# Kernel optimization log

Measured on AMD Instinct MI355X. Metric: run time of the kernel, lower is better.

The kernel has to match this reference:

```python
import jax, jax.numpy as jnp
import numpy as np
from jax import lax

B, DIM, H, W = 2, 128, 192, 192
GS = [16, 32, 32, 48]          # group ratios [1,2,2,3]/8 of DIM
HID = int(DIM * 2.66)          # 340, Restormer-style hidden width


def _pool_mat(n_in, n_out):
    # torch AdaptiveAvgPool as an explicit linear map [n_out, n_in]
    P = np.zeros((n_out, n_in), np.float32)
    for o in range(n_out):
        s = (o * n_in) // n_out
        e = ((o + 1) * n_in + n_out - 1) // n_out
        P[o, s:e] = 1.0 / (e - s)
    return jnp.asarray(P)


def _ln(t, w, b):
    # WithBias LayerNorm over the channel dim of NCHW (== LN over last dim of b(hw)c)
    mu = t.mean(1, keepdims=True)
    var = ((t - mu) ** 2).mean(1, keepdims=True)
    return (t - mu) / jnp.sqrt(var + 1e-5) * w[None, :, None, None] + b[None, :, None, None]


def _c1x1(t, w):
    return jnp.einsum('oc,bchw->bohw', w, t)


def _dw3(t, w):
    return lax.conv_general_dilated(t, w, (1, 1), 'SAME',
                                    dimension_numbers=('NCHW', 'OIHW', 'NCHW'),
                                    feature_group_count=t.shape[1])


def _c1d(t, w, b):
    return jnp.einsum('oc,bcl->bol', w, t) + b[None, :, None]


def _gelu(t):
    return jax.nn.gelu(t, approximate=False)


def _forward(x, qv_cache, ln1_w, ln1_b, ln2_w, ln2_b, temperature, w_qkv, w_qkv_dw, w_proj,
             intra_down_w, intra_down_b, intra_up_w, intra_up_b, intra_gate_w, intra_gate_b,
             inter0_cw_w, inter0_cw_b, inter0_g_w, inter0_g_b,
             inter1_cw_w, inter1_cw_b, inter1_g_w, inter1_g_b,
             inter2_cw_w, inter2_cw_b, inter2_g_w, inter2_g_b,
             inter3_cw_w, inter3_cw_b, inter3_g_w, inter3_g_b,
             ffn_in_w, ffn_dw_w, ffn_out_w):
    b, c, h, w_ = x.shape
    hw = h * w_
    inter_p = [(inter0_cw_w, inter0_cw_b, inter0_g_w, inter0_g_b),
               (inter1_cw_w, inter1_cw_b, inter1_g_w, inter1_g_b),
               (inter2_cw_w, inter2_cw_b, inter2_g_w, inter2_g_b),
               (inter3_cw_w, inter3_cw_b, inter3_g_w, inter3_g_b)]
    # ---- attention branch ----
    xn = _ln(x, ln1_w, ln1_b)
    qkv = _dw3(_c1x1(xn, w_qkv), w_qkv_dw)
    q, k, v = jnp.split(qkv, 3, axis=1)
    q = q.reshape(b, c, hw); k = k.reshape(b, c, hw); v = v.reshape(b, c, hw)
    # correlation-based channel re-grouping (torch.corrcoef on batch-mean of q)
    cf = q.mean(0)                                   # [C, HW]
    xm = cf - cf.mean(1, keepdims=True)
    cov = xm @ xm.T
    dsd = jnp.sqrt(jnp.diagonal(cov))
    corr = cov / (dsd[:, None] * dsd[None, :])
    idx = jnp.argsort(-corr.mean(1))                 # descending mean similarity
    q = q[:, idx]; k = k[:, idx]; v = v[:, idx]
    atts, tmpc, outs = [], [], []
    start = 0
    for i, g in enumerate(GS):
        qg = q[:, start:start + g]; kg = k[:, start:start + g]; vg = v[:, start:start + g]
        start += g
        qn = qg / jnp.maximum(jnp.linalg.norm(qg, axis=-1, keepdims=True), 1e-12)
        kn = kg / jnp.maximum(jnp.linalg.norm(kg, axis=-1, keepdims=True), 1e-12)
        att = jax.nn.softmax(jnp.einsum('bcl,bdl->bcd', qn, kn) * temperature[i, 0, 0], axis=-1)
        tmpc.append(lax.stop_gradient(qn) + lax.stop_gradient(kn))
        # Inter_CacheModulation: adaptive-pool cache to [g,g], FiLM + gated conv1d
        cw_w, cw_b, g_w, g_b = inter_p[i]
        P = _pool_mat(c, g)
        aligned = jnp.einsum('oi,bij,pj->bop', P, qv_cache, P)    # [1, g, g]
        scale, shift = jnp.split(_c1d(aligned + att, cw_w, cw_b), 2, axis=1)
        x1p = att * scale + shift
        att = x1p * _gelu(_c1d(x1p, g_w, g_b)) + att
        atts.append(att)
        outs.append(jnp.einsum('bcd,bdl->bcl', att, vg))
    # CalculateCurrentLayerCache: resize each group's batch-mean attn to [C,C].
    # Original does (u * c_i) // dim with c_i == dim, i.e. elementwise floor.
    acc = jnp.zeros((1, c, c), x.dtype)
    for a in atts:
        m = lax.stop_gradient(a).mean(0, keepdims=True)[:, None]  # [1,1,g,g]
        u = jax.image.resize(m, (1, 1, c, c), method='bilinear')
        acc = acc + jnp.floor(u)[:, 0]
    qv_new = qv_cache * 0.9 + acc * 0.1
    out_all = jnp.concatenate(outs, axis=1)          # [B, C, HW]
    tmp_all = jnp.concatenate(tmpc, axis=1)
    # Intra_CacheModulation
    s = tmp_all + out_all
    gated = _gelu(_c1d(s, intra_gate_w, intra_gate_b)) * s
    out_all = _c1d(_c1d(gated, intra_down_w, intra_down_b), intra_up_w, intra_up_b) + out_all
    x1 = x + _c1x1(out_all.reshape(b, c, h, w_), w_proj)
    # ---- gated-dconv FFN ----
    xn2 = _ln(x1, ln2_w, ln2_b)
    y1, y2 = jnp.split(_dw3(_c1x1(xn2, ffn_in_w), ffn_dw_w), 2, axis=1)
    out = x1 + _c1x1(_gelu(y1) * y2, ffn_out_w)
    return out, qv_new


def setup_inputs() -> dict:
    key = jax.random.key(0)
    ks = jax.random.split(key, 40)
    def w(i, shape, s=0.02):
        return jax.random.normal(ks[i], shape, jnp.float32) * s
    p = {}
    p['x'] = jax.random.normal(ks[0], (B, DIM, H, W), jnp.float32)
    p['qv_cache'] = jax.random.uniform(ks[1], (1, DIM, DIM), jnp.float32)
    p['ln1_w'] = jnp.ones((DIM,), jnp.float32); p['ln1_b'] = jnp.zeros((DIM,), jnp.float32)
    p['ln2_w'] = jnp.ones((DIM,), jnp.float32); p['ln2_b'] = jnp.zeros((DIM,), jnp.float32)
    p['temperature'] = jnp.ones((4, 1, 1), jnp.float32)
    p['w_qkv'] = w(2, (3 * DIM, DIM))
    p['w_qkv_dw'] = w(3, (3 * DIM, 1, 3, 3))
    p['w_proj'] = w(4, (DIM, DIM))
    p['intra_down_w'] = w(5, (DIM // 2, DIM)); p['intra_down_b'] = jnp.zeros((DIM // 2,), jnp.float32)
    p['intra_up_w'] = w(6, (DIM, DIM // 2)); p['intra_up_b'] = jnp.zeros((DIM,), jnp.float32)
    p['intra_gate_w'] = w(7, (DIM, DIM)); p['intra_gate_b'] = jnp.zeros((DIM,), jnp.float32)
    for i, g in enumerate(GS):
        p[f'inter{i}_cw_w'] = w(8 + 2 * i, (2 * g, g))
        p[f'inter{i}_cw_b'] = jnp.zeros((2 * g,), jnp.float32)
        p[f'inter{i}_g_w'] = w(9 + 2 * i, (g, g))
        p[f'inter{i}_g_b'] = jnp.zeros((g,), jnp.float32)
    p['ffn_in_w'] = w(20, (2 * HID, DIM))
    p['ffn_dw_w'] = w(21, (2 * HID, 1, 3, 3))
    p['ffn_out_w'] = w(22, (DIM, HID))
    return p


def reference(x, qv_cache, ln1_w, ln1_b, ln2_w, ln2_b, temperature, w_qkv, w_qkv_dw, w_proj,
              intra_down_w, intra_down_b, intra_up_w, intra_up_b, intra_gate_w, intra_gate_b,
              inter0_cw_w, inter0_cw_b, inter0_g_w, inter0_g_b,
              inter1_cw_w, inter1_cw_b, inter1_g_w, inter1_g_b,
              inter2_cw_w, inter2_cw_b, inter2_g_w, inter2_g_b,
              inter3_cw_w, inter3_cw_b, inter3_g_w, inter3_g_b,
              ffn_in_w, ffn_dw_w, ffn_out_w):
    return _forward(x, qv_cache, ln1_w, ln1_b, ln2_w, ln2_b, temperature, w_qkv, w_qkv_dw, w_proj,
                    intra_down_w, intra_down_b, intra_up_w, intra_up_b, intra_gate_w, intra_gate_b,
                    inter0_cw_w, inter0_cw_b, inter0_g_w, inter0_g_b,
                    inter1_cw_w, inter1_cw_b, inter1_g_w, inter1_g_b,
                    inter2_cw_w, inter2_cw_b, inter2_g_w, inter2_g_b,
                    inter3_cw_w, inter3_cw_b, inter3_g_w, inter3_g_b,
                    ffn_in_w, ffn_dw_w, ffn_out_w)
```

## Files before the change

### kernel.cpp

```cpp
#include <hip/hip_runtime.h>
#include <math.h>

#define TPB 256

constexpr int BN_  = 2;
constexpr int CDIM = 128;
constexpr int HH   = 192;
constexpr int WW   = 192;
constexpr int HWc  = HH * WW;
constexpr int C3   = 384;
constexpr int HID  = 340;
constexpr int NL2  = 288;
constexpr int CH2  = HWc / NL2;
constexpr int CV   = 288;

typedef unsigned short bf16_t;
typedef __attribute__((ext_vector_type(8))) __bf16 bf16x8;
typedef __attribute__((ext_vector_type(4))) float f32x4;

__device__ __forceinline__ float b2f(bf16_t v) {
  unsigned u = ((unsigned)v) << 16;
  return __uint_as_float(u);
}
__device__ __forceinline__ bf16_t f2b(float f) {
  unsigned u = __float_as_uint(f);
  unsigned r = (u + 0x7FFFu + ((u >> 16) & 1u)) >> 16;
  return (bf16_t)r;
}
__device__ __forceinline__ float ldf(const float* p) { return *p; }
__device__ __forceinline__ float ldf(const bf16_t* p) { return b2f(*p); }
__device__ __forceinline__ void stf(float* p, float v) { *p = v; }
__device__ __forceinline__ void stf(bf16_t* p, float v) { *p = f2b(v); }

__device__ __forceinline__ void ldv4(const float* p, float* v) {
  float4 t = *(const float4*)p;
  v[0] = t.x; v[1] = t.y; v[2] = t.z; v[3] = t.w;
}
__device__ __forceinline__ void ldv4(const bf16_t* p, float* v) {
  ushort4 t = *(const ushort4*)p;
  v[0] = b2f(t.x); v[1] = b2f(t.y); v[2] = b2f(t.z); v[3] = b2f(t.w);
}
__device__ __forceinline__ void stv4(float* p, const float* v) {
  float4 t; t.x = v[0]; t.y = v[1]; t.z = v[2]; t.w = v[3];
  *(float4*)p = t;
}
__device__ __forceinline__ void stv4(bf16_t* p, const float* v) {
  ushort4 t; t.x = f2b(v[0]); t.y = f2b(v[1]); t.z = f2b(v[2]); t.w = f2b(v[3]);
  *(ushort4*)p = t;
}

__device__ __forceinline__ float gelu_f(float x) {
  return 0.5f * x * (1.0f + erff(x * 0.7071067811865475f));
}

__device__ __forceinline__ void unpack8(uint4 v, float* rv) {
  unsigned wv[4] = {v.x, v.y, v.z, v.w};
#pragma unroll
  for (int j = 0; j < 8; ++j)
    rv[j + 1] = b2f((bf16_t)((wv[j >> 1] >> ((j & 1) * 16)) & 0xFFFFu));
}
__device__ __forceinline__ uint4 pack8(const float* a) {
  uint4 o;
  unsigned w[4];
#pragma unroll
  for (int p = 0; p < 4; ++p) {
    unsigned lo = f2b(a[2 * p]), hi = f2b(a[2 * p + 1]);
    w[p] = lo | (hi << 16);
  }
  o.x = w[0]; o.y = w[1]; o.z = w[2]; o.w = w[3];
  return o;
}
__device__ __forceinline__ float sum8(uint4 v) {
  unsigned w[4] = {v.x, v.y, v.z, v.w};
  float s = 0.f;
#pragma unroll
  for (int j = 0; j < 8; ++j)
    s += b2f((bf16_t)((w[j >> 1] >> ((j & 1) * 16)) & 0xFFFFu));
  return s;
}
__device__ __forceinline__ float sumsq8(uint4 v) {
  unsigned w[4] = {v.x, v.y, v.z, v.w};
  float s = 0.f;
#pragma unroll
  for (int j = 0; j < 8; ++j) {
    float t = b2f((bf16_t)((w[j >> 1] >> ((j & 1) * 16)) & 0xFFFFu));
    s += t * t;
  }
  return s;
}

__device__ __constant__ int dGSZ[4]   = {16, 32, 32, 48};
__device__ __constant__ int dGST[4]   = {0, 16, 48, 80};
__device__ __constant__ int dAOFF[4]  = {0, 256, 1280, 2304};
__device__ __constant__ int dABASE[4] = {0, 512, 2560, 4608};

constexpr size_t oATTRAW  = 0;
constexpr size_t oATTS2   = 65536;
constexpr size_t oMUP     = 102400;
constexpr size_t oWB      = 131072;
constexpr size_t oATTS    = 1327104;
constexpr size_t oNORMQ   = 1363968;
constexpr size_t oNORMK   = 1364992;
constexpr size_t oIDX     = 1366016;
constexpr size_t oMU      = 1366528;
constexpr size_t oCOV     = 1367040;
constexpr size_t oQKV     = 1572864;
constexpr size_t oXN      = 58195968;
constexpr size_t oOUTALL  = 77070336;
constexpr size_t oSBUF    = 95944704;
constexpr size_t WS_NEED  = 114819072;
constexpr size_t oCHUNK1  = oOUTALL;
constexpr size_t oCOVPART = oOUTALL;
constexpr size_t oCOVP2   = oSBUF;
constexpr size_t oQKPART  = oXN;
constexpr size_t oGATED   = oQKV;
constexpr size_t oDBUF    = oQKV + 18874368;
constexpr size_t oY0C     = oOUTALL;
constexpr size_t oZ       = oQKV;
constexpr size_t oX1B     = oXN;

constexpr int eWQ   = 0;
constexpr int eGATE = 49152;
constexpr int eDOWN = 65536;
constexpr int eUP   = 73728;
constexpr int ePROJ = 81920;
constexpr int eFFI  = 98304;
constexpr int eFFO  = 185344;
constexpr int eTOT  = 234496;

__global__ __launch_bounds__(TPB) void k_wcvt(const float* __restrict__ wq,
                                              const float* __restrict__ gate,
                                              const float* __restrict__ down,
                                              const float* __restrict__ up,
                                              const float* __restrict__ proj,
                                              const float* __restrict__ ffi,
                                              const float* __restrict__ ffo,
                                              bf16_t* __restrict__ wb) {
  int t = blockIdx.x * TPB + threadIdx.x;
  if (t >= eTOT) return;
  int u = t;
  if (u < 49152) { wb[eWQ + u] = f2b(wq[u]); return; }
  u -= 49152;
  if (u < 16384) { wb[eGATE + u] = f2b(gate[u]); return; }
  u -= 16384;
  if (u < 8192)  { wb[eDOWN + u] = f2b(down[u]); return; }
  u -= 8192;
  if (u < 8192)  { wb[eUP + u] = f2b(up[u]); return; }
  u -= 8192;
  if (u < 16384) { wb[ePROJ + u] = f2b(proj[u]); return; }
  u -= 16384;
  if (u < 87040) { wb[eFFI + u] = f2b(ffi[u]); return; }
  u -= 87040;
  {
    int o = u / 384, k = u - o * 384;
    wb[eFFO + u] = (k < HID) ? f2b(ffo[o * HID + k]) : (bf16_t)0;
  }
}

template <typename TI>
__global__ __launch_bounds__(TPB) void k_ln(const TI* __restrict__ x,
                                            const float* __restrict__ w,
                                            const float* __restrict__ bias,
                                            bf16_t* __restrict__ out) {
  int t = blockIdx.x * TPB + threadIdx.x;
  if (t >= BN_ * HWc) return;
  int b = t / HWc, l = t - b * HWc;
  const TI* xb = x + (size_t)b * CDIM * HWc + l;
  float s = 0.f, s2 = 0.f;
#pragma unroll 4
  for (int c = 0; c < CDIM; ++c) { float v = ldf(&xb[(size_t)c * HWc]); s += v; s2 += v * v; }
  float mu  = s * (1.f / CDIM);
  float var = s2 * (1.f / CDIM) - mu * mu;
  float inv = 1.f / sqrtf(var + 1e-5f);
  bf16_t* ob = out + (size_t)b * CDIM * HWc + l;
#pragma unroll 4
  for (int c = 0; c < CDIM; ++c)
    stf(&ob[(size_t)c * HWc], (ldf(&xb[(size_t)c * HWc]) - mu) * inv * w[c] + bias[c]);
}

template <typename TO, typename TA, int KT, int EPI>
__global__ __launch_bounds__(TPB) void k_mgA(const bf16_t* __restrict__ W,
                                             const bf16_t* __restrict__ W2, int osplit,
                                             const float* __restrict__ bias,
                                             const bf16_t* __restrict__ in,
                                             const TA* __restrict__ aux,
                                             TO* __restrict__ out, int O,
                                             int ibr, int obr, int abr) {
  constexpr int L  = HWc;
  constexpr int PK = KT + 8;
  constexpr int KH = KT / 2;
  constexpr int SH = (KT == 128) ? 6 : 5;
  __shared__ bf16_t At[128 * PK];
  __shared__ bf16_t Wt[64 * PK];
  int b = blockIdx.y;
  const bf16_t* inb  = in  + (size_t)b * ibr * L;
  const TA*     auxb = aux ? aux + (size_t)b * abr * L : nullptr;
  TO*           outb = out + (size_t)b * obr * L;
  int l0 = blockIdx.x * 128;
  int tid = threadIdx.x, lane = tid & 63, wid = tid >> 6;
  int wm = wid >> 1, wn = wid & 1;
  int cl = lane & 15, rg = lane >> 4;

#pragma unroll
  for (int r = 0; r < (KH * 16) / TPB; ++r) {
    int u  = tid + r * TPB;
    int k2 = u & (KH - 1), lb = u >> SH;
    int ka = k2 * 2;
    uint4 rowA = *(const uint4*)(&inb[(size_t)ka * L + l0 + lb * 8]);
    uint4 rowB = *(const uint4*)(&inb[(size_t)(ka + 1) * L + l0 + lb * 8]);
    unsigned wa[4] = {rowA.x, rowA.y, rowA.z, rowA.w};
    unsigned wb[4] = {rowB.x, rowB.y, rowB.z, rowB.w};
#pragma unroll
    for (int j = 0; j < 8; ++j) {
      unsigned va = (wa[j >> 1] >> ((j & 1) * 16)) & 0xFFFFu;
      unsigned vb = (wb[j >> 1] >> ((j & 1) * 16)) & 0xFFFFu;
      *(unsigned*)(&At[(lb * 8 + j) * PK + ka]) = va | (vb << 16);
    }
  }

  int noc = (O + 63) >> 6;
  for (int oc = 0; oc < noc; ++oc) {
    int o0 = oc * 64;
#pragma unroll
    for (int r = 0; r < (64 * KT / 8) / TPB; ++r) {
      int e = tid + r * TPB;
      int o = e / (KT / 8), k8 = (e % (KT / 8)) * 8;
      int og = o0 + o;
      uint4 wv = {0u, 0u, 0u, 0u};
      if (og < O) {
        const bf16_t* wrow = (og < osplit) ? (W + (size_t)og * KT)
                                           : (W2 + (size_t)(og - osplit) * KT);
        wv = *(const uint4*)(&wrow[k8]);
      }
      *(uint4*)(&Wt[o * PK + k8]) = wv;
    }
    __syncthreads();
    f32x4 acc[2][4];
#pragma unroll
    for (int m = 0; m < 2; ++m)
#pragma unroll
      for (int n = 0; n < 4; ++n) acc[m][n] = (f32x4){0.f, 0.f, 0.f, 0.f};
#pragma unroll
    for (int kk = 0; kk < KT / 32; ++kk) {
      int kof = kk * 32 + rg * 8;
      bf16x8 a[2], bfr[4];
#pragma unroll
      for (int m = 0; m < 2; ++m)
        a[m] = *(const bf16x8*)(&Wt[(wm * 32 + m * 16 + cl) * PK + kof]);
#pragma unroll
      for (int n = 0; n < 4; ++n)
        bfr[n] = *(const bf16x8*)(&At[(wn * 64 + n * 16 + cl) * PK + kof]);
#pragma unroll
      for (int m = 0; m < 2; ++m)
#pragma unroll
        for (int n = 0; n < 4; ++n)
          acc[m][n] = __builtin_amdgcn_mfma_f32_16x16x32_bf16(bfr[n], a[m], acc[m][n], 0, 0, 0);
    }
    __syncthreads();
#pragma unroll
    for (int m = 0; m < 2; ++m) {
      int og = o0 + wm * 32 + m * 16 + cl;
      if (og >= O) continue;
      float bv = bias ? bias[og] : 0.f;
#pragma unroll
      for (int n = 0; n < 4; ++n) {
        int lcol = l0 + wn * 64 + n * 16 + rg * 4;
        size_t off = (size_t)og * L + lcol;
        float v[4];
#pragma unroll
        for (int r = 0; r < 4; ++r) v[r] = acc[m][n][r] + bv;
        if (EPI == 1) {
          float a4[4]; ldv4(&auxb[off], a4);
#pragma unroll
          for (int r = 0; r < 4; ++r) v[r] += a4[r];
        } else if (EPI == 2) {
          float a4[4]; ldv4(&auxb[off], a4);
#pragma unroll
          for (int r = 0; r < 4; ++r) v[r] = gelu_f(v[r]) * a4[r];
        }
        stv4(&outb[off], v);
      }
    }
  }
}

template <typename TO, typename TA, int EPI>
__global__ __launch_bounds__(TPB) void k_mgB(const bf16_t* __restrict__ Wb,
                                             const float* __restrict__ bias,
                                             const bf16_t* __restrict__ in,
                                             const TA* __restrict__ aux,
                                             TO* __restrict__ out, int O, int K,
                                             int ibr, int obr, int abr) {
  constexpr int L = HWc;
  constexpr int PK = 72, BK = 64, WSTR = 384;
  __shared__ bf16_t At[128 * PK];
  __shared__ bf16_t Wt[128 * PK];
  int b = blockIdx.y;
  const bf16_t* inb  = in  + (size_t)b * ibr * L;
  const TA*     auxb = aux ? aux + (size_t)b * abr * L : nullptr;
  TO*           outb = out + (size_t)b * obr * L;
  int l0 = blockIdx.x * 128;
  int tid = threadIdx.x, lane = tid & 63, wid = tid >> 6;
  int wm = wid >> 1, wn = wid & 1;
  int cl = lane & 15, rg = lane >> 4;

  f32x4 acc[4][4];
#pragma unroll
  for (int m = 0; m < 4; ++m)
#pragma unroll
    for (int n = 0; n < 4; ++n) acc[m][n] = (f32x4){0.f, 0.f, 0.f, 0.f};

  for (int k0 = 0; k0 < K; k0 += BK) {
#pragma unroll
    for (int r = 0; r < 2; ++r) {
      int u = tid + r * TPB;
      int k2 = u & 31, lb = u >> 5;
      int ka = k0 + k2 * 2;
      uint4 rowA = {0u,0u,0u,0u}, rowB = {0u,0u,0u,0u};
      if (ka < K)     rowA = *(const uint4*)(&inb[(size_t)ka * L + l0 + lb * 8]);
      if (ka + 1 < K) rowB = *(const uint4*)(&inb[(size_t)(ka + 1) * L + l0 + lb * 8]);
      unsigned wa[4] = {rowA.x, rowA.y, rowA.z, rowA.w};
      unsigned wb[4] = {rowB.x, rowB.y, rowB.z, rowB.w};
#pragma unroll
      for (int j = 0; j < 8; ++j) {
        unsigned va = (wa[j >> 1] >> ((j & 1) * 16)) & 0xFFFFu;
        unsigned vb = (wb[j >> 1] >> ((j & 1) * 16)) & 0xFFFFu;
        *(unsigned*)(&At[(lb * 8 + j) * PK + k2 * 2]) = va | (vb << 16);
      }
    }
#pragma unroll
    for (int r = 0; r < 4; ++r) {
      int e = tid + r * TPB;
      int o = e >> 3, k8 = (e & 7) * 8;
      uint4 wv = *(const uint4*)(&Wb[(size_t)o * WSTR + k0 + k8]);
      *(uint4*)(&Wt[o * PK + k8]) = wv;
    }
    __syncthreads();
#pragma unroll
    for (int kk = 0; kk < 2; ++kk) {
      int kof = kk * 32 + rg * 8;
      bf16x8 a[4], bfr[4];
#pragma unroll
      for (int m = 0; m < 4; ++m)
        a[m] = *(const bf16x8*)(&Wt[(wm * 64 + m * 16 + cl) * PK + kof]);
#pragma unroll
      for (int n = 0; n < 4; ++n)
        bfr[n] = *(const bf16x8*)(&At[(wn * 64 + n * 16 + cl) * PK + kof]);
#pragma unroll
      for (int m = 0; m < 4; ++m)
#pragma unroll
        for (int n = 0; n < 4; ++n)
          acc[m][n] = __builtin_amdgcn_mfma_f32_16x16x32_bf16(bfr[n], a[m], acc[m][n], 0, 0, 0);
    }
    __syncthreads();
  }
#pragma unroll
  for (int m = 0; m < 4; ++m) {
    int og = wm * 64 + m * 16 + cl;
    if (og >= O) continue;
    float bv = bias ? bias[og] : 0.f;
#pragma unroll
    for (int n = 0; n < 4; ++n) {
      int lcol = l0 + wn * 64 + n * 16 + rg * 4;
      size_t off = (size_t)og * L + lcol;
      float v[4];
#pragma unroll
      for (int r = 0; r < 4; ++r) v[r] = acc[m][n][r] + bv;
      if (EPI == 1) {
        float a4[4]; ldv4(&auxb[off], a4);
#pragma unroll
        for (int r = 0; r < 4; ++r) v[r] += a4[r];
      } else if (EPI == 2) {
        float a4[4]; ldv4(&auxb[off], a4);
#pragma unroll
        for (int r = 0; r < 4; ++r) v[r] = gelu_f(v[r]) * a4[r];
      }
      stv4(&outb[off], v);
    }
  }
}

__global__ __launch_bounds__(TPB) void k_dw3v(const bf16_t* __restrict__ in,
                                              const float* __restrict__ wt,
                                              bf16_t* __restrict__ out,
                                              int Cc, int c0, int CoutTotal, long totalG) {
  long t = (long)blockIdx.x * TPB + threadIdx.x;
  if (t >= totalG) return;
  int g = (int)(t % (HWc / 8));
  long bc = t / (HWc / 8);
  int cl = (int)(bc % Cc);
  int b = (int)(bc / Cc);
  int h = g / (WW / 8), w8 = (g % (WW / 8)) * 8;
  const bf16_t* ib = in + ((size_t)b * Cc + cl) * HWc;
  const float* wc = wt + (size_t)(c0 + cl) * 9;
  float rowv[3][10];
#pragma unroll
  for (int dy = -1; dy <= 1; ++dy) {
    float* rv = rowv[dy + 1];
    int hh = h + dy;
    if ((unsigned)hh >= (unsigned)HH) {
#pragma unroll
      for (int j = 0; j < 10; ++j) rv[j] = 0.f;
      continue;
    }
    const bf16_t* rp = ib + hh * WW + w8;
    unpack8(*(const uint4*)rp, rv);
    rv[0] = (w8 > 0) ? b2f(rp[-1]) : 0.f;
    rv[9] = (w8 + 8 < WW) ? b2f(rp[8]) : 0.f;
  }
  float a[8];
#pragma unroll
  for (int j = 0; j < 8; ++j) {
    float s = 0.f;
#pragma unroll
    for (int dy = 0; dy < 3; ++dy)
#pragma unroll
      for (int dx = 0; dx < 3; ++dx)
        s += rowv[dy][j + dx] * wc[dy * 3 + dx];
    a[j] = s;
  }
  *(uint4*)(&out[((size_t)b * CoutTotal + c0 + cl) * HWc + h * WW + w8]) = pack8(a);
}

__global__ __launch_bounds__(TPB) void k_mu1(const bf16_t* __restrict__ qkv,
                                             float* __restrict__ mupart) {
  int c = blockIdx.x, ch = blockIdx.y;
  int tid = threadIdx.x;
  int base = ch * (HWc / 8);
  __shared__ float red[TPB];
  float s = 0.f;
  for (int u = tid; u < (HWc / 8) / 8; u += TPB) {
    uint4 v0 = *(const uint4*)(&qkv[(size_t)c * HWc + base + u * 8]);
    uint4 v1 = *(const uint4*)(&qkv[(size_t)C3 * HWc + (size_t)c * HWc + base + u * 8]);
    s += 0.5f * (sum8(v0) + sum8(v1));
  }
  red[tid] = s;
  __syncthreads();
  for (int st = TPB / 2; st > 0; st >>= 1) {
    if (tid < st) red[tid] += red[tid + st];
    __syncthreads();
  }
  if (tid == 0) mupart[c * 8 + ch] = red[0];
}
__global__ __launch_bounds__(CDIM) void k_mured(const float* __restrict__ mupart,
                                                float* __restrict__ mu) {
  int c = threadIdx.x;
  float s = 0.f;
#pragma unroll
  for (int ch = 0; ch < 8; ++ch) s += mupart[c * 8 + ch];
  mu[c] = s / HWc;
}

__global__ __launch_bounds__(TPB) void k_cov4(const bf16_t* __restrict__ qkv,
                                              float* __restrict__ part) {
  constexpr int PK = 136;
  __shared__ bf16_t Xt[128 * PK];
  int chunk = blockIdx.x;
  int base = chunk * 128;
  int tid = threadIdx.x, lane = tid & 63, wid = tid >> 6;
  int wm = wid >> 1, wn = wid & 1;
  int cl = lane & 15, rg = lane >> 4;
#pragma unroll
  for (int r = 0; r < 8; ++r) {
    int u = tid + r * TPB;
    int c = u >> 4, l8 = (u & 15) * 8;
    uint4 v0 = *(const uint4*)(&qkv[(size_t)c * HWc + base + l8]);
    uint4 v1 = *(const uint4*)(&qkv[(size_t)C3 * HWc + (size_t)c * HWc + base + l8]);
    unsigned w0[4] = {v0.x, v0.y, v0.z, v0.w};
    unsigned w1[4] = {v1.x, v1.y, v1.z, v1.w};
    float cf[8];
#pragma unroll
    for (int j = 0; j < 8; ++j) {
      float a = b2f((bf16_t)((w0[j >> 1] >> ((j & 1) * 16)) & 0xFFFFu));
      float bq = b2f((bf16_t)((w1[j >> 1] >> ((j & 1) * 16)) & 0xFFFFu));
      cf[j] = 0.5f * (a + bq);
    }
    *(uint4*)(&Xt[c * PK + l8]) = pack8(cf);
  }
  __syncthreads();
  f32x4 acc[4][4];
#pragma unroll
  for (int m = 0; m < 4; ++m)
#pragma unroll
    for (int n = 0; n < 4; ++n) acc[m][n] = (f32x4){0.f, 0.f, 0.f, 0.f};
#pragma unroll
  for (int kk = 0; kk < 4; ++kk) {
    int kof = kk * 32 + rg * 8;
    bf16x8 a[4], bfr[4];
#pragma unroll
    for (int m = 0; m < 4; ++m)
      a[m] = *(const bf16x8*)(&Xt[(wm * 64 + m * 16 + cl) * PK + kof]);
#pragma unroll
    for (int n = 0; n < 4; ++n)
      bfr[n] = *(const bf16x8*)(&Xt[(wn * 64 + n * 16 + cl) * PK + kof]);
#pragma unroll
    for (int m = 0; m < 4; ++m)
#pragma unroll
      for (int n = 0; n < 4; ++n)
        acc[m][n] = __builtin_amdgcn_mfma_f32_16x16x32_bf16(bfr[n], a[m], acc[m][n], 0, 0, 0);
  }
  float* pb = part + (size_t)chunk * CDIM * CDIM;
#pragma unroll
  for (int m = 0; m < 4; ++m) {
    int c = wm * 64 + m * 16 + cl;
#pragma unroll
    for (int n = 0; n < 4; ++n) {
      int d0 = wn * 64 + n * 16 + rg * 4;
      float v[4] = {acc[m][n][0], acc[m][n][1], acc[m][n][2], acc[m][n][3]};
      stv4(&pb[c * CDIM + d0], v);
    }
  }
}

__global__ __launch_bounds__(TPB) void k_covred1(const float* __restrict__ part,
                                                 float* __restrict__ p2) {
  int t = blockIdx.x * TPB + threadIdx.x;
  int yg = blockIdx.y;
  float s = 0.f;
  for (int p = yg * 36; p < (yg + 1) * 36; ++p)
    s += part[(size_t)p * CDIM * CDIM + t];
  p2[(size_t)yg * CDIM * CDIM + t] = s;
}
__global__ __launch_bounds__(TPB) void k_covred2(const float* __restrict__ p2,
                                                 const float* __restrict__ mu,
                                                 float* __restrict__ cov) {
  int t = blockIdx.x * TPB + threadIdx.x;
  if (t >= CDIM * CDIM) return;
  float s = 0.f;
#pragma unroll
  for (int y = 0; y < 8; ++y) s += p2[(size_t)y * CDIM * CDIM + t];
  int c = t >> 7, d = t & 127;
  cov[t] = s - (float)HWc * mu[c] * mu[d];
}

__global__ __launch_bounds__(CDIM) void k_rank(const float* __restrict__ cov,
                                               int* __restrict__ idx) {
  __shared__ float dsd[CDIM], score[CDIM];
  int tid = threadIdx.x;
  dsd[tid] = sqrtf(cov[tid * CDIM + tid]);
  __syncthreads();
  {
    float s = 0.f, di = dsd[tid];
    for (int d = 0; d < CDIM; ++d) s += cov[tid * CDIM + d] / (di * dsd[d]);
    score[tid] = s;
  }
  __syncthreads();
  {
    float my = score[tid];
    int rank = 0;
    for (int d = 0; d < CDIM; ++d)
      rank += (score[d] > my) || (score[d] == my && d < tid);
    idx[rank] = tid;
  }
}

__global__ __launch_bounds__(TPB) void k_norms(const bf16_t* __restrict__ qkv,
                                               const int* __restrict__ idx,
                                               float* __restrict__ normq,
                                               float* __restrict__ normk) {
  int p = blockIdx.x, b = blockIdx.y, which = blockIdx.z;
  int ch = idx[p] + which * CDIM;
  const bf16_t* row = qkv + ((size_t)b * C3 + ch) * HWc;
  __shared__ float red[TPB];
  float s = 0.f;
  for (int u = threadIdx.x; u < HWc / 8; u += TPB)
    s += sumsq8(*(const uint4*)(&row[u * 8]));
  red[threadIdx.x] = s;
  __syncthreads();
  for (int st = TPB / 2; st > 0; st >>= 1) {
    if (threadIdx.x < st) red[threadIdx.x] += red[threadIdx.x + st];
    __syncthreads();
  }
  if (threadIdx.x == 0) {
    float n = fmaxf(sqrtf(red[0]), 1e-12f);
    (which ? normk : normq)[b * CDIM + p] = n;
  }
}

template <int G>
__global__ __launch_bounds__(TPB) void k_qk2(const bf16_t* __restrict__ qkv,
                                             const int* __restrict__ idx, int start,
                                             float* __restrict__ partial) {
  constexpr int RT = G / 16;
  constexpr int U  = G * CH2 / 8;
  int nl = blockIdx.x, b = blockIdx.y;
  __shared__ float qs[G][CH2 + 2], ks[G][CH2 + 2];
  __shared__ int idxg[G];
  int tid = threadIdx.x;
  if (tid < G) idxg[tid] = idx[start + tid];
  __syncthreads();
  int l0 = nl * CH2;
  for (int u = tid; u < U; u += TPB) {
    int r = u / (CH2 / 8), c8 = (u % (CH2 / 8)) * 8;
    int ch = idxg[r];
    uint4 vq = *(const uint4*)(&qkv[((size_t)b * C3 + ch) * HWc + l0 + c8]);
    uint4 vk = *(const uint4*)(&qkv[((size_t)b * C3 + CDIM + ch) * HWc + l0 + c8]);
    unsigned wq[4] = {vq.x, vq.y, vq.z, vq.w};
    unsigned wk[4] = {vk.x, vk.y, vk.z, vk.w};
#pragma unroll
    for (int j = 0; j < 8; ++j) {
      qs[r][c8 + j] = b2f((bf16_t)((wq[j >> 1] >> ((j & 1) * 16)) & 0xFFFFu));
      ks[r][c8 + j] = b2f((bf16_t)((wk[j >> 1] >> ((j & 1) * 16)) & 0xFFFFu));
    }
  }
  __syncthreads();
  int ti = tid & 15, tj = tid >> 4;
  float acc[RT][RT];
#pragma unroll
  for (int m = 0; m < RT; ++m)
#pragma unroll
    for (int n = 0; n < RT; ++n) acc[m][n] = 0.f;
#pragma unroll 4
  for (int l = 0; l < CH2; ++l) {
    float qa[RT], kb[RT];
#pragma unroll
    for (int m = 0; m < RT; ++m) qa[m] = qs[ti * RT + m][l];
#pragma unroll
    for (int n = 0; n < RT; ++n) kb[n] = ks[tj * RT + n][l];
#pragma unroll
    for (int m = 0; m < RT; ++m)
#pragma unroll
      for (int n = 0; n < RT; ++n) acc[m][n] += qa[m] * kb[n];
  }
  float* pb = partial + ((size_t)(b * NL2) + nl) * G * G;
#pragma unroll
  for (int m = 0; m < RT; ++m)
#pragma unroll
    for (int n = 0; n < RT; ++n)
      pb[(ti * RT + m) * G + tj * RT + n] = acc[m][n];
}

__global__ __launch_bounds__(TPB) void k_qkredg(const float* __restrict__ qkpart,
                                                float* __restrict__ attraw) {
  int t = blockIdx.x * TPB + threadIdx.x;
  if (t >= BN_ * 4608) return;
  int b = t / 4608, e = t - b * 4608;
  int gi = (e < 256) ? 0 : (e < 1280) ? 1 : (e < 2304) ? 2 : 3;
  const int gg4[4]    = {256, 1024, 1024, 2304};
  const int pgoff[4]  = {0, 147456, 737280, 1327104};
  const int aoff4[4]  = {0, 256, 1280, 2304};
  int GGg = gg4[gi];
  int el = e - aoff4[gi];
  const float* pb = qkpart + pgoff[gi] + (size_t)(b * NL2) * GGg + el;
  float s = 0.f;
  for (int nl = 0; nl < NL2; ++nl) s += pb[(size_t)nl * GGg];
  attraw[t] = s;
}

__global__ __launch_bounds__(TPB) void k_smg(const float* __restrict__ attraw,
                                             const float* __restrict__ normq,
                                             const float* __restrict__ normk,
                                             const float* __restrict__ temperature,
                                             float* __restrict__ attS) {
  int b = blockIdx.x, gi = blockIdx.y;
  int G = dGSZ[gi], start = dGST[gi];
  int GG = G * G;
  const float* ar = attraw + b * 4608 + dAOFF[gi];
  float* as = attS + b * 4608 + dAOFF[gi];
  float temp = temperature[gi];
  __shared__ float att[2304];
  int tid = threadIdx.x;
  for (int e = tid; e < GG; e += TPB) {
    int i = e / G, j = e - i * G;
    att[e] = ar[e] * temp / (normq[b * CDIM + start + i] * normk[b * CDIM + start + j]);
  }
  __syncthreads();
  if (tid < G) {
    float mx = -3.4e38f;
    for (int j = 0; j < G; ++j) mx = fmaxf(mx, att[tid * G + j]);
    float ssum = 0.f;
    for (int j = 0; j < G; ++j) { float ex = expf(att[tid * G + j] - mx); att[tid * G + j] = ex; ssum += ex; }
    float inv = 1.f / ssum;
    for (int j = 0; j < G; ++j) att[tid * G + j] *= inv;
  }
  __syncthreads();
  for (int e = tid; e < GG; e += TPB) as[e] = att[e];
}

__global__ __launch_bounds__(TPB) void k_imlpg(const float* __restrict__ attS,
                                               const float* __restrict__ qv_cache,
                                               const float* __restrict__ cw0, const float* __restrict__ cb0,
                                               const float* __restrict__ gw0, const float* __restrict__ gb0,
                                               const float* __restrict__ cw1, const float* __restrict__ cb1,
                                               const float* __restrict__ gw1, const float* __restrict__ gb1,
                                               const float* __restrict__ cw2, const float* __restrict__ cb2,
                                               const float* __restrict__ gw2, const float* __restrict__ gb2,
                                               const float* __restrict__ cw3, const float* __restrict__ cb3,
                                               const float* __restrict__ gw3, const float* __restrict__ gb3,
                                               float* __restrict__ attF) {
  int b = blockIdx.x, gi = blockIdx.y, tile = blockIdx.z;
  int G = dGSZ[gi];
  int p0 = tile * 16;
  if (p0 >= G) return;
  int GG = G * G;
  const float* cw_w = (gi == 0) ? cw0 : (gi == 1) ? cw1 : (gi == 2) ? cw2 : cw3;
  const float* cw_b = (gi == 0) ? cb0 : (gi == 1) ? cb1 : (gi == 2) ? cb2 : cb3;
  const float* g_w  = (gi == 0) ? gw0 : (gi == 1) ? gw1 : (gi == 2) ? gw2 : gw3;
  const float* g_b  = (gi == 0) ? gb0 : (gi == 1) ? gb1 : (gi == 2) ? gb2 : gb3;
  const float* as = attS + b * 4608 + dAOFF[gi];
  float* af = attF + dABASE[gi] + (size_t)b * GG;
  int tid = threadIdx.x;
  __shared__ float cwW[2 * 48 * 48];
  __shared__ float gW[48 * 48];
  __shared__ float attC[48 * 16], t1C[48 * 16], scC[48 * 16], shC[48 * 16],
                   x1pC[48 * 16], t2C[48 * 16];
  for (int e = tid; e < 2 * G * G; e += TPB) cwW[e] = cw_w[e];
  for (int e = tid; e < G * G; e += TPB) gW[e] = g_w[e];
  for (int u = tid; u < G * 16; u += TPB) {
    int c = u >> 4, pl = u & 15;
    int p = p0 + pl;
    float av = 0.f, pv = 0.f;
    if (p < G) {
      av = as[c * G + p];
      int so = c * CDIM / G, eo = ((c + 1) * CDIM + G - 1) / G;
      int sp = p * CDIM / G, ep = ((p + 1) * CDIM + G - 1) / G;
      float ssum = 0.f;
      for (int i2 = so; i2 < eo; ++i2)
        for (int j2 = sp; j2 < ep; ++j2) ssum += qv_cache[i2 * CDIM + j2];
      pv = ssum / (float)((eo - so) * (ep - sp));
    }
    attC[u] = av;
    t1C[u] = pv + av;
  }
  __syncthreads();
  for (int u = tid; u < 2 * G * 16; u += TPB) {
    int o = u >> 4, pl = u & 15;
    float acc = cw_b[o];
    for (int c = 0; c < G; ++c) acc += cwW[o * G + c] * t1C[c * 16 + pl];
    if (o < G) scC[o * 16 + pl] = acc;
    else       shC[(o - G) * 16 + pl] = acc;
  }
  __syncthreads();
  for (int u = tid; u < G * 16; u += TPB)
    x1pC[u] = attC[u] * scC[u] + shC[u];
  __syncthreads();
  for (int u = tid; u < G * 16; u += TPB) {
    int o = u >> 4, pl = u & 15;
    float acc = g_b[o];
    for (int c = 0; c < G; ++c) acc += gW[o * G + c] * x1pC[c * 16 + pl];
    t2C[u] = acc;
  }
  __syncthreads();
  for (int u = tid; u < G * 16; u += TPB) {
    int c = u >> 4, pl = u & 15;
    int p = p0 + pl;
    if (p < G)
      af[c * G + p] = x1pC[u] * gelu_f(t2C[u]) + attC[u];
  }
}

template <int G>
__global__ __launch_bounds__(TPB) void k_av(const bf16_t* __restrict__ qkv,
                                            const int* __restrict__ idx,
                                            const float* __restrict__ attF,
                                            const float* __restrict__ normq,
                                            const float* __restrict__ normk, int start,
                                            bf16_t* __restrict__ out_all,
                                            bf16_t* __restrict__ s_buf) {
  constexpr int GH = G / 2;
  int b = blockIdx.y;
  int l0 = blockIdx.x * 128;
  __shared__ float vt[G][129];
  __shared__ float attL[G * G];
  __shared__ int idxg[G];
  int tid = threadIdx.x;
  if (tid < G) idxg[tid] = idx[start + tid];
  for (int e = tid; e < G * G; e += TPB) attL[e] = attF[(size_t)b * G * G + e];
  __syncthreads();
  for (int e = tid; e < G * 128; e += TPB) {
    int j = e >> 7, c = e & 127;
    vt[j][c] = b2f(qkv[((size_t)b * C3 + 2 * CDIM + idxg[j]) * HWc + l0 + c]);
  }
  __syncthreads();
  int ll = tid & 127, half = tid >> 7;
  float acc[GH];
#pragma unroll
  for (int i = 0; i < GH; ++i) acc[i] = 0.f;
  for (int j = 0; j < G; ++j) {
    float vv = vt[j][ll];
#pragma unroll
    for (int i = 0; i < GH; ++i) acc[i] += attL[(half * GH + i) * G + j] * vv;
  }
#pragma unroll
  for (int i = 0; i < GH; ++i) {
    int ig = half * GH + i;
    int p = start + ig;
    int ch = idxg[ig];
    float qv = b2f(qkv[((size_t)b * C3 + ch) * HWc + l0 + ll]);
    float kv = b2f(qkv[((size_t)b * C3 + CDIM + ch) * HWc + l0 + ll]);
    float tmp = qv / normq[b * CDIM + p] + kv / normk[b * CDIM + p];
    size_t off = ((size_t)b * CDIM + p) * HWc + l0 + ll;
    stf(&out_all[off], acc[i]);
    stf(&s_buf[off], acc[i] + tmp);
  }
}

__global__ __launch_bounds__(TPB) void k_qvnew(const float* __restrict__ attsF,
                                               const float* __restrict__ qv_cache,
                                               float* __restrict__ out_qv) {
  int t = blockIdx.x * TPB + threadIdx.x;
  if (t >= CDIM * CDIM) return;
  int r = t >> 7, cq = t & 127;
  const int gs[4]   = {16, 32, 32, 48};
  const int base[4] = {0, 512, 2560, 4608};
  float acc = 0.f;
  for (int gi = 0; gi < 4; ++gi) {
    int g = gs[gi], gg = g * g;
    const float* a0 = attsF + base[gi];
    float scale = (float)g / CDIM;
    float fr = (r + 0.5f) * scale - 0.5f;
    float fc = (cq + 0.5f) * scale - 0.5f;
    float flr = floorf(fr), flc = floorf(fc);
    int i0 = (int)flr, j0 = (int)flc;
    float wr = fr - flr, wcw = fc - flc;
    int i0c = max(i0, 0), i1c = min(i0 + 1, g - 1);
    int j0c = max(j0, 0), j1c = min(j0 + 1, g - 1);
    float m00 = 0.5f * (a0[i0c * g + j0c] + a0[gg + i0c * g + j0c]);
    float m01 = 0.5f * (a0[i0c * g + j1c] + a0[gg + i0c * g + j1c]);
    float m10 = 0.5f * (a0[i1c * g + j0c] + a0[gg + i1c * g + j0c]);
    float m11 = 0.5f * (a0[i1c * g + j1c] + a0[gg + i1c * g + j1c]);
    float val = (1.f - wr) * ((1.f - wcw) * m00 + wcw * m01)
              + wr * ((1.f - wcw) * m10 + wcw * m11);
    acc += floorf(val);
  }
  out_qv[t] = qv_cache[t] * 0.9f + acc * 0.1f;
}

__global__ __launch_bounds__(TPB) void k_dwgeluv(const bf16_t* __restrict__ y0c,
                                                 const float* __restrict__ wt,
                                                 bf16_t* __restrict__ z,
                                                 int Cc, int c0, long totalG) {
  long t = (long)blockIdx.x * TPB + threadIdx.x;
  if (t >= totalG) return;
  int g = (int)(t % (HWc / 8));
  long bc = t / (HWc / 8);
  int cl = (int)(bc % Cc);
  int b = (int)(bc / Cc);
  int h = g / (WW / 8), w8 = (g % (WW / 8)) * 8;
  const bf16_t* i1 = y0c + ((size_t)b * 2 * Cc + cl) * HWc;
  const bf16_t* i2 = y0c + ((size_t)b * 2 * Cc + Cc + cl) * HWc;
  const float* w1 = wt + (size_t)(c0 + cl) * 9;
  const float* w2 = wt + (size_t)(HID + c0 + cl) * 9;
  float r1[3][10], r2[3][10];
#pragma unroll
  for (int dy = -1; dy <= 1; ++dy) {
    float* v1 = r1[dy + 1];
    float* v2 = r2[dy + 1];
    int hh = h + dy;
    if ((unsigned)hh >= (unsigned)HH) {
#pragma unroll
      for (int j = 0; j < 10; ++j) { v1[j] = 0.f; v2[j] = 0.f; }
      continue;
    }
    const bf16_t* p1 = i1 + hh * WW + w8;
    const bf16_t* p2 = i2 + hh * WW + w8;
    unpack8(*(const uint4*)p1, v1);
    unpack8(*(const uint4*)p2, v2);
    bool hasL = (w8 > 0), hasR = (w8 + 8 < WW);
    v1[0] = hasL ? b2f(p1[-1]) : 0.f;
    v1[9] = hasR ? b2f(p1[8]) : 0.f;
    v2[0] = hasL ? b2f(p2[-1]) : 0.f;
    v2[9] = hasR ? b2f(p2[8]) : 0.f;
  }
  float o[8];
#pragma unroll
  for (int j = 0; j < 8; ++j) {
    float a1 = 0.f, a2 = 0.f;
#pragma unroll
    for (int dy = 0; dy < 3; ++dy)
#pragma unroll
      for (int dx = 0; dx < 3; ++dx) {
        a1 += r1[dy][j + dx] * w1[dy * 3 + dx];
        a2 += r2[dy][j + dx] * w2[dy * 3 + dx];
      }
    o[j] = gelu_f(a1) * a2;
  }
  *(uint4*)(&z[((size_t)b * HID + c0 + cl) * HWc + h * WW + w8]) = pack8(o);
}

extern "C" void kernel_launch(void* const* d_in, const int* in_sizes, int n_in,
                              void* d_out, int out_size, void* d_ws, size_t ws_size,
                              hipStream_t stream) {
  if (ws_size < WS_NEED) return;

  const float* x        = (const float*)d_in[0];
  const float* qv_cache = (const float*)d_in[1];
  const float* ln1_w    = (const float*)d_in[2];
  const float* ln1_b    = (const float*)d_in[3];
  const float* ln2_w    = (const float*)d_in[4];
  const float* ln2_b    = (const float*)d_in[5];
  const float* temperature = (const float*)d_in[6];
  const float* w_qkv    = (const float*)d_in[7];
  const float* w_qkv_dw = (const float*)d_in[8];
  const float* w_proj   = (const float*)d_in[9];
  const float* intra_down_w = (const float*)d_in[10];
  const float* intra_down_b = (const float*)d_in[11];
  const float* intra_up_w   = (const float*)d_in[12];
  const float* intra_up_b   = (const float*)d_in[13];
  const float* intra_gate_w = (const float*)d_in[14];
  const float* intra_gate_b = (const float*)d_in[15];
  const float* ffn_in_w  = (const float*)d_in[32];
  const float* ffn_dw_w  = (const float*)d_in[33];
  const float* ffn_out_w = (const float*)d_in[34];

  char* wsb = (char*)d_ws;
  float* out    = (float*)d_out;
  float* out_qv = out + (size_t)BN_ * CDIM * HWc;
  bf16_t* xn2   = (bf16_t*)d_out;

  float*  attraw  = (float*)(wsb + oATTRAW);
  float*  attS    = (float*)(wsb + oATTS2);
  float*  mupart  = (float*)(wsb + oMUP);
  bf16_t* wb      = (bf16_t*)(wsb + oWB);
  float*  atts    = (float*)(wsb + oATTS);
  float*  normq   = (float*)(wsb + oNORMQ);
  float*  normk   = (float*)(wsb + oNORMK);
  int*    idx     = (int*)(wsb + oIDX);
  float*  mu      = (float*)(wsb + oMU);
  float*  cov     = (float*)(wsb + oCOV);
  bf16_t* qkv     = (bf16_t*)(wsb + oQKV);
  bf16_t* xn      = (bf16_t*)(wsb + oXN);
  bf16_t* out_all = (bf16_t*)(wsb + oOUTALL);
  bf16_t* sbuf    = (bf16_t*)(wsb + oSBUF);
  bf16_t* chunk1  = (bf16_t*)(wsb + oCHUNK1);
  float*  covpart = (float*)(wsb + oCOVPART);
  float*  covp2   = (float*)(wsb + oCOVP2);
  float*  qkpart  = (float*)(wsb + oQKPART);
  bf16_t* gated   = (bf16_t*)(wsb + oGATED);
  bf16_t* dbuf    = (bf16_t*)(wsb + oDBUF);
  bf16_t* x1b     = (bf16_t*)(wsb + oX1B);
  bf16_t* y0c     = (bf16_t*)(wsb + oY0C);
  bf16_t* zbuf    = (bf16_t*)(wsb + oZ);

  const bf16_t* wq_b   = wb + eWQ;
  const bf16_t* gate_b = wb + eGATE;
  const bf16_t* down_b = wb + eDOWN;
  const bf16_t* up_b   = wb + eUP;
  const bf16_t* proj_b = wb + ePROJ;
  const bf16_t* ffi_b  = wb + eFFI;
  const bf16_t* ffo_b  = wb + eFFO;

  const int GX = HWc / 128;
  const int NOS = 1 << 30;
  dim3 gA(GX, BN_);
  const int pgoff[4] = {0, 147456, 737280, 1327104};

  k_wcvt<<<(eTOT + TPB - 1) / TPB, TPB, 0, stream>>>(
      w_qkv, intra_gate_w, intra_down_w, intra_up_w, w_proj, ffn_in_w, ffn_out_w, wb);

  k_ln<float><<<(BN_ * HWc + TPB - 1) / TPB, TPB, 0, stream>>>(x, ln1_w, ln1_b, xn);

  for (int ci = 0; ci < 2; ++ci) {
    int c0 = ci * 192;
    k_mgA<bf16_t, float, 128, 0><<<gA, TPB, 0, stream>>>(
        wq_b + (size_t)c0 * CDIM, wq_b, NOS, nullptr, xn, nullptr, chunk1,
        192, CDIM, 192, 0);
    long totG = (long)BN_ * 192 * (HWc / 8);
    k_dw3v<<<(unsigned)((totG + TPB - 1) / TPB), TPB, 0, stream>>>(
        chunk1, w_qkv_dw, qkv, 192, c0, C3, totG);
  }

  k_mu1<<<dim3(CDIM, 8), TPB, 0, stream>>>(qkv, mupart);
  k_mured<<<1, CDIM, 0, stream>>>(mupart, mu);
  k_cov4<<<CV, TPB, 0, stream>>>(qkv, covpart);
  k_covred1<<<dim3(64, 8), TPB, 0, stream>>>(covpart, covp2);
  k_covred2<<<64, TPB, 0, stream>>>(covp2, mu, cov);
  k_rank<<<1, CDIM, 0, stream>>>(cov, idx);
  k_norms<<<dim3(CDIM, BN_, 2), TPB, 0, stream>>>(qkv, idx, normq, normk);

  k_qk2<16><<<dim3(NL2, BN_), TPB, 0, stream>>>(qkv, idx, 0,  qkpart + pgoff[0]);
  k_qk2<32><<<dim3(NL2, BN_), TPB, 0, stream>>>(qkv, idx, 16, qkpart + pgoff[1]);
  k_qk2<32><<<dim3(NL2, BN_), TPB, 0, stream>>>(qkv, idx, 48, qkpart + pgoff[2]);
  k_qk2<48><<<dim3(NL2, BN_), TPB, 0, stream>>>(qkv, idx, 80, qkpart + pgoff[3]);
  k_qkredg<<<(BN_ * 4608 + TPB - 1) / TPB, TPB, 0, stream>>>(qkpart, attraw);
  k_smg<<<dim3(BN_, 4), TPB, 0, stream>>>(attraw, normq, normk, temperature, attS);
  k_imlpg<<<dim3(BN_, 4, 3), TPB, 0, stream>>>(
      attS, qv_cache,
      (const float*)d_in[16], (const float*)d_in[17], (const float*)d_in[18], (const float*)d_in[19],
      (const float*)d_in[20], (const float*)d_in[21], (const float*)d_in[22], (const float*)d_in[23],
      (const float*)d_in[24], (const float*)d_in[25], (const float*)d_in[26], (const float*)d_in[27],
      (const float*)d_in[28], (const float*)d_in[29], (const float*)d_in[30], (const float*)d_in[31],
      atts);
  k_av<16><<<dim3(HWc / 128, BN_), TPB, 0, stream>>>(qkv, idx, atts + 0,    normq, normk, 0,  out_all, sbuf);
  k_av<32><<<dim3(HWc / 128, BN_), TPB, 0, stream>>>(qkv, idx, atts + 512,  normq, normk, 16, out_all, sbuf);
  k_av<32><<<dim3(HWc / 128, BN_), TPB, 0, stream>>>(qkv, idx, atts + 2560, normq, normk, 48, out_all, sbuf);
  k_av<48><<<dim3(HWc / 128, BN_), TPB, 0, stream>>>(qkv, idx, atts + 4608, normq, normk, 80, out_all, sbuf);
  k_qvnew<<<(CDIM * CDIM + TPB - 1) / TPB, TPB, 0, stream>>>(atts, qv_cache, out_qv);

  k_mgA<bf16_t, bf16_t, 128, 2><<<gA, TPB, 0, stream>>>(
      gate_b, gate_b, NOS, intra_gate_b, sbuf, sbuf, gated,
      CDIM, CDIM, CDIM, CDIM);
  k_mgA<bf16_t, float, 128, 0><<<gA, TPB, 0, stream>>>(
      down_b, down_b, NOS, intra_down_b, gated, nullptr, dbuf,
      CDIM / 2, CDIM, CDIM / 2, 0);
  k_mgA<bf16_t, bf16_t, 64, 1><<<gA, TPB, 0, stream>>>(
      up_b, up_b, NOS, intra_up_b, dbuf, out_all, out_all,
      CDIM, CDIM / 2, CDIM, CDIM);
  k_mgA<bf16_t, float, 128, 1><<<gA, TPB, 0, stream>>>(
      proj_b, proj_b, NOS, nullptr, out_all, x, x1b, CDIM, CDIM, CDIM, CDIM);
  k_ln<bf16_t><<<(BN_ * HWc + TPB - 1) / TPB, TPB, 0, stream>>>(x1b, ln2_w, ln2_b, xn2);

  for (int ci = 0; ci < 4; ++ci) {
    int c0 = ci * 85;
    k_mgA<bf16_t, float, 128, 0><<<gA, TPB, 0, stream>>>(
        ffi_b + (size_t)c0 * CDIM, ffi_b + (size_t)(HID + c0) * CDIM, 85,
        nullptr, xn2, nullptr, y0c, 170, CDIM, 170, 0);
    long totG = (long)BN_ * 85 * (HWc / 8);
    k_dwgeluv<<<(unsigned)((totG + TPB - 1) / TPB), TPB, 0, stream>>>(
        y0c, ffn_dw_w, zbuf, 85, c0, totG);
  }
  k_mgB<float, bf16_t, 1><<<gA, TPB, 0, stream>>>(
      ffo_b, nullptr, zbuf, x1b, out, CDIM, HID, HID, CDIM, CDIM);
}
```

Measured before the change: 605.3 us.

## Merge grouped qk/av launches, reuse shared tile in gate epilogue, widen FFN chunks

The four per-group qk and av kernels are each merged into one launch that dispatches on blockIdx.z and uses dynamic shared memory. The gate GEMM gets a new epilogue that reads its multiplicand from the A tile already held in shared memory, so the aux input no longer has to be reloaded from global memory. The FFN input projection and depthwise-GELU stage now run in 2 chunks instead of 4, with the y0c and z buffers swapped to make room. The goals are fewer launches and tail gaps and less redundant global traffic. The cost is that every merged block reserves the largest group's shared memory, which can lower occupancy.

```diff
diff --git a/kernel.cpp b/kernel.cpp
--- a/kernel.cpp
+++ b/kernel.cpp
@@ -115,8 +115,8 @@
 constexpr size_t oQKPART  = oXN;
 constexpr size_t oGATED   = oQKV;
 constexpr size_t oDBUF    = oQKV + 18874368;
-constexpr size_t oY0C     = oOUTALL;
-constexpr size_t oZ       = oQKV;
+constexpr size_t oY0C     = oQKV;
+constexpr size_t oZ       = oOUTALL;
 constexpr size_t oX1B     = oXN;
 
 constexpr int eWQ   = 0;
@@ -277,6 +277,11 @@
           float a4[4]; ldv4(&auxb[off], a4);
 #pragma unroll
           for (int r = 0; r < 4; ++r) v[r] = gelu_f(v[r]) * a4[r];
+        } else if (EPI == 3) {
+          int lloc = wn * 64 + n * 16 + rg * 4;
+#pragma unroll
+          for (int r = 0; r < 4; ++r)
+            v[r] = gelu_f(v[r]) * b2f(At[(lloc + r) * PK + og]);
         }
         stv4(&outb[off], v);
       }
@@ -578,14 +583,14 @@
 }
 
 template <int G>
-__global__ __launch_bounds__(TPB) void k_qk2(const bf16_t* __restrict__ qkv,
-                                             const int* __restrict__ idx, int start,
-                                             float* __restrict__ partial) {
+__device__ __forceinline__ void qk2_impl(char* sm, const bf16_t* __restrict__ qkv,
+                                         const int* __restrict__ idx, int start,
+                                         float* __restrict__ partial, int nl, int b) {
   constexpr int RT = G / 16;
   constexpr int U  = G * CH2 / 8;
-  int nl = blockIdx.x, b = blockIdx.y;
-  __shared__ float qs[G][CH2 + 2], ks[G][CH2 + 2];
-  __shared__ int idxg[G];
+  float (*qs)[CH2 + 2] = (float (*)[CH2 + 2])sm;
+  float (*ks)[CH2 + 2] = (float (*)[CH2 + 2])(sm + (size_t)G * (CH2 + 2) * 4);
+  int* idxg = (int*)(sm + (size_t)2 * G * (CH2 + 2) * 4);
   int tid = threadIdx.x;
   if (tid < G) idxg[tid] = idx[start + tid];
   __syncthreads();
@@ -628,6 +633,17 @@
 #pragma unroll
     for (int n = 0; n < RT; ++n)
       pb[(ti * RT + m) * G + tj * RT + n] = acc[m][n];
+}
+
+__global__ __launch_bounds__(TPB) void k_qk2g(const bf16_t* __restrict__ qkv,
+                                              const int* __restrict__ idx,
+                                              float* __restrict__ qkpart) {
+  extern __shared__ char sm[];
+  int nl = blockIdx.x, b = blockIdx.y, gi = blockIdx.z;
+  if (gi == 0)      qk2_impl<16>(sm, qkv, idx, 0,  qkpart + 0,       nl, b);
+  else if (gi == 1) qk2_impl<32>(sm, qkv, idx, 16, qkpart + 147456,  nl, b);
+  else if (gi == 2) qk2_impl<32>(sm, qkv, idx, 48, qkpart + 737280,  nl, b);
+  else              qk2_impl<48>(sm, qkv, idx, 80, qkpart + 1327104, nl, b);
 }
 
 __global__ __launch_bounds__(TPB) void k_qkredg(const float* __restrict__ qkpart,
@@ -750,19 +766,17 @@
 }
 
 template <int G>
-__global__ __launch_bounds__(TPB) void k_av(const bf16_t* __restrict__ qkv,
-                                            const int* __restrict__ idx,
-                                            const float* __restrict__ attF,
-                                            const float* __restrict__ normq,
-                                            const float* __restrict__ normk, int start,
-                                            bf16_t* __restrict__ out_all,
-                                            bf16_t* __restrict__ s_buf) {
+__device__ __forceinline__ void av_impl(char* sm, const bf16_t* __restrict__ qkv,
+                                        const int* __restrict__ idx,
+                                        const float* __restrict__ attF,
+                                        const float* __restrict__ normq,
+                                        const float* __restrict__ normk, int start,
+                                        bf16_t* __restrict__ out_all,
+                                        bf16_t* __restrict__ s_buf, int l0, int b) {
   constexpr int GH = G / 2;
-  int b = blockIdx.y;
-  int l0 = blockIdx.x * 128;
-  __shared__ float vt[G][129];
-  __shared__ float attL[G * G];
-  __shared__ int idxg[G];
+  float (*vt)[129] = (float (*)[129])sm;
+  float* attL = (float*)(sm + (size_t)G * 129 * 4);
+  int* idxg = (int*)(sm + (size_t)G * 129 * 4 + (size_t)G * G * 4);
   int tid = threadIdx.x;
   if (tid < G) idxg[tid] = idx[start + tid];
   for (int e = tid; e < G * G; e += TPB) attL[e] = attF[(size_t)b * G * G + e];
@@ -793,6 +807,21 @@
     stf(&out_all[off], acc[i]);
     stf(&s_buf[off], acc[i] + tmp);
   }
+}
+
+__global__ __launch_bounds__(TPB) void k_avg(const bf16_t* __restrict__ qkv,
+                                             const int* __restrict__ idx,
+                                             const float* __restrict__ atts,
+                                             const float* __restrict__ normq,
+                                             const float* __restrict__ normk,
+                                             bf16_t* __restrict__ out_all,
+                                             bf16_t* __restrict__ s_buf) {
+  extern __shared__ char sm[];
+  int l0 = blockIdx.x * 128, b = blockIdx.y, gi = blockIdx.z;
+  if (gi == 0)      av_impl<16>(sm, qkv, idx, atts + 0,    normq, normk, 0,  out_all, s_buf, l0, b);
+  else if (gi == 1) av_impl<32>(sm, qkv, idx, atts + 512,  normq, normk, 16, out_all, s_buf, l0, b);
+  else if (gi == 2) av_impl<32>(sm, qkv, idx, atts + 2560, normq, normk, 48, out_all, s_buf, l0, b);
+  else              av_impl<48>(sm, qkv, idx, atts + 4608, normq, normk, 80, out_all, s_buf, l0, b);
 }
 
 __global__ __launch_bounds__(TPB) void k_qvnew(const float* __restrict__ attsF,
@@ -943,7 +972,6 @@
   const int GX = HWc / 128;
   const int NOS = 1 << 30;
   dim3 gA(GX, BN_);
-  const int pgoff[4] = {0, 147456, 737280, 1327104};
 
   k_wcvt<<<(eTOT + TPB - 1) / TPB, TPB, 0, stream>>>(
       w_qkv, intra_gate_w, intra_down_w, intra_up_w, w_proj, ffn_in_w, ffn_out_w, wb);
@@ -968,10 +996,10 @@
   k_rank<<<1, CDIM, 0, stream>>>(cov, idx);
   k_norms<<<dim3(CDIM, BN_, 2), TPB, 0, stream>>>(qkv, idx, normq, normk);
 
-  k_qk2<16><<<dim3(NL2, BN_), TPB, 0, stream>>>(qkv, idx, 0,  qkpart + pgoff[0]);
-  k_qk2<32><<<dim3(NL2, BN_), TPB, 0, stream>>>(qkv, idx, 16, qkpart + pgoff[1]);
-  k_qk2<32><<<dim3(NL2, BN_), TPB, 0, stream>>>(qkv, idx, 48, qkpart + pgoff[2]);
-  k_qk2<48><<<dim3(NL2, BN_), TPB, 0, stream>>>(qkv, idx, 80, qkpart + pgoff[3]);
+  {
+    size_t dyn = (size_t)2 * 48 * (CH2 + 2) * 4 + 48 * 4;
+    k_qk2g<<<dim3(NL2, BN_, 4), TPB, dyn, stream>>>(qkv, idx, qkpart);
+  }
   k_qkredg<<<(BN_ * 4608 + TPB - 1) / TPB, TPB, 0, stream>>>(qkpart, attraw);
   k_smg<<<dim3(BN_, 4), TPB, 0, stream>>>(attraw, normq, normk, temperature, attS);
   k_imlpg<<<dim3(BN_, 4, 3), TPB, 0, stream>>>(
@@ -981,15 +1009,16 @@
       (const float*)d_in[24], (const float*)d_in[25], (const float*)d_in[26], (const float*)d_in[27],
       (const float*)d_in[28], (const float*)d_in[29], (const float*)d_in[30], (const float*)d_in[31],
       atts);
-  k_av<16><<<dim3(HWc / 128, BN_), TPB, 0, stream>>>(qkv, idx, atts + 0,    normq, normk, 0,  out_all, sbuf);
-  k_av<32><<<dim3(HWc / 128, BN_), TPB, 0, stream>>>(qkv, idx, atts + 512,  normq, normk, 16, out_all, sbuf);
-  k_av<32><<<dim3(HWc / 128, BN_), TPB, 0, stream>>>(qkv, idx, atts + 2560, normq, normk, 48, out_all, sbuf);
-  k_av<48><<<dim3(HWc / 128, BN_), TPB, 0, stream>>>(qkv, idx, atts + 4608, normq, normk, 80, out_all, sbuf);
+  {
+    size_t dyn = (size_t)48 * 129 * 4 + (size_t)48 * 48 * 4 + 48 * 4;
+    k_avg<<<dim3(HWc / 128, BN_, 4), TPB, dyn, stream>>>(
+        qkv, idx, atts, normq, normk, out_all, sbuf);
+  }
   k_qvnew<<<(CDIM * CDIM + TPB - 1) / TPB, TPB, 0, stream>>>(atts, qv_cache, out_qv);
 
-  k_mgA<bf16_t, bf16_t, 128, 2><<<gA, TPB, 0, stream>>>(
-      gate_b, gate_b, NOS, intra_gate_b, sbuf, sbuf, gated,
-      CDIM, CDIM, CDIM, CDIM);
+  k_mgA<bf16_t, float, 128, 3><<<gA, TPB, 0, stream>>>(
+      gate_b, gate_b, NOS, intra_gate_b, sbuf, nullptr, gated,
+      CDIM, CDIM, CDIM, 0);
   k_mgA<bf16_t, float, 128, 0><<<gA, TPB, 0, stream>>>(
       down_b, down_b, NOS, intra_down_b, gated, nullptr, dbuf,
       CDIM / 2, CDIM, CDIM / 2, 0);
@@ -1000,14 +1029,14 @@
       proj_b, proj_b, NOS, nullptr, out_all, x, x1b, CDIM, CDIM, CDIM, CDIM);
   k_ln<bf16_t><<<(BN_ * HWc + TPB - 1) / TPB, TPB, 0, stream>>>(x1b, ln2_w, ln2_b, xn2);
 
-  for (int ci = 0; ci < 4; ++ci) {
-    int c0 = ci * 85;
+  for (int ci = 0; ci < 2; ++ci) {
+    int c0 = ci * 170;
     k_mgA<bf16_t, float, 128, 0><<<gA, TPB, 0, stream>>>(
-        ffi_b + (size_t)c0 * CDIM, ffi_b + (size_t)(HID + c0) * CDIM, 85,
-        nullptr, xn2, nullptr, y0c, 170, CDIM, 170, 0);
-    long totG = (long)BN_ * 85 * (HWc / 8);
+        ffi_b + (size_t)c0 * CDIM, ffi_b + (size_t)(HID + c0) * CDIM, 170,
+        nullptr, xn2, nullptr, y0c, 340, CDIM, 340, 0);
+    long totG = (long)BN_ * 170 * (HWc / 8);
     k_dwgeluv<<<(unsigned)((totG + TPB - 1) / TPB), TPB, 0, stream>>>(
-        y0c, ffn_dw_w, zbuf, 85, c0, totG);
+        y0c, ffn_dw_w, zbuf, 170, c0, totG);
   }
   k_mgB<float, bf16_t, 1><<<gA, TPB, 0, stream>>>(
       ffo_b, nullptr, zbuf, x1b, out, CDIM, HID, HID, CDIM, CDIM);
```

Result: faster. 541.6 us (-10.5%).
